# Optimization experiments

Measured on AMD Instinct MI355X. Metric: run time of the kernel, lower is better.

## Reference

```python
import jax, jax.numpy as jnp
import numpy as np

B, N, C = 512, 200, 512
NH, WS = 8, 5  # num_heads, window size (window_size=(5,1), W=1 so w-axis is trivial)
HD = C // NH
SCALE = HD ** -0.5


def setup_inputs() -> dict:
    key = jax.random.key(0)
    k0, k1, k2 = jax.random.split(key, 3)
    std = C ** -0.5
    return {
        "x": jax.random.normal(k0, (B, N, C), dtype=jnp.float32),
        "qkv_w": jax.random.normal(k1, (C, 3 * C), dtype=jnp.float32) * std,
        "qkv_b": jnp.zeros((3 * C,), dtype=jnp.float32),
        "proj_w": jax.random.normal(k2, (C, C), dtype=jnp.float32) * std,
        "proj_b": jnp.zeros((C,), dtype=jnp.float32),
    }


def reference(x, qkv_w, qkv_b, proj_w, proj_b):
    b, n, c = x.shape
    g = n // WS  # number of windows along the 200-token axis (w_group == 1)
    # window partition: since W=1 and window_size[1]=1, partition is a pure reshape
    xw = x.reshape(b * g, WS, c)
    qkv = xw @ qkv_w + qkv_b                      # [b*g, WS, 3C]
    qkv = qkv.reshape(b * g, WS, 3, NH, HD)
    q, k, v = jnp.moveaxis(qkv, 2, 0)             # each [b*g, WS, NH, HD]
    q = jnp.swapaxes(q, 1, 2)                     # [b*g, NH, WS, HD]
    k = jnp.swapaxes(k, 1, 2)
    v = jnp.swapaxes(v, 1, 2)
    attn = jnp.einsum("gnqd,gnkd->gnqk", q, k) * SCALE
    attn = jax.nn.softmax(attn, axis=-1)
    o = jnp.einsum("gnqk,gnkd->gnqd", attn, v)    # [b*g, NH, WS, HD]
    o = jnp.swapaxes(o, 1, 2).reshape(b, n, c)    # window reverse (pure reshape)
    return o @ proj_w + proj_b
```

## Files before the change

kernel.cpp:

```cpp
#include <hip/hip_runtime.h>
#include <stdint.h>


typedef unsigned short u16;
typedef __bf16 bf16_t;
typedef bf16_t bf16x8 __attribute__((ext_vector_type(8)));
typedef float f32x4 __attribute__((ext_vector_type(4)));
typedef u16 u16x8 __attribute__((ext_vector_type(8)));

__device__ __forceinline__ float b2f(u16 u) {
  return __uint_as_float(((uint32_t)u) << 16);
}
__device__ __forceinline__ u16 f2b(float f) {
  uint32_t u = __float_as_uint(f);
  u += 0x7FFFu + ((u >> 16) & 1u);
  return (u16)(u >> 16);
}

#define GLOAD_LDS16(g, l)                                     \
  __builtin_amdgcn_global_load_lds(                           \
      (const __attribute__((address_space(1))) void*)(g),     \
      (__attribute__((address_space(3))) void*)(l), 16, 0, 0)

__global__ void k_sniff_bias(const uint32_t* __restrict__ x,
                             const void* __restrict__ qb,
                             const void* __restrict__ pb,
                             uint32_t* __restrict__ flag,
                             u16* __restrict__ bq, u16* __restrict__ bp) {
  __shared__ uint32_t fsh;
  if (threadIdx.x == 0) {
    int cnt = 0;
    for (int i = 0; i < 256; ++i) {
      uint32_t e = (x[i] >> 23) & 0xFFu;
      if (e >= 64u && e <= 192u) ++cnt;
    }
    uint32_t fl = (cnt >= 128) ? 1u : 0u;
    *flag = fl;
    fsh = fl;
  }
  __syncthreads();
  const bool f = fsh != 0;
  for (int i = threadIdx.x; i < 2048; i += 1024) {
    if (i < 1536)
      bq[i] = f ? f2b(((const float*)qb)[i]) : ((const u16*)qb)[i];
    else {
      int j = i - 1536;
      bp[j] = f ? f2b(((const float*)pb)[j]) : ((const u16*)pb)[j];
    }
  }
}

__global__ void k_prep_w2(const void* __restrict__ qkvw,
                          const void* __restrict__ projw,
                          u16* __restrict__ wq, u16* __restrict__ wp,
                          const uint32_t* __restrict__ flag) {
  __shared__ u16 tile[32][33];
  const bool f = (*flag) != 0;
  int bxi = blockIdx.x;
  const void* in;
  u16* out;
  int Cc;
  if (bxi < 48) {
    in = qkvw; out = wq; Cc = 1536;
  } else {
    bxi -= 48; in = projw; out = wp; Cc = 512;
  }
  const int R = 512;
  const int bx = bxi * 32, by = blockIdx.y * 32;
  const int tx = threadIdx.x, ty = threadIdx.y;
  for (int i = ty; i < 32; i += 8) {
    size_t idx = (size_t)(by + i) * Cc + bx + tx;
    tile[i][tx] = f ? f2b(((const float*)in)[idx]) : ((const u16*)in)[idx];
  }
  __syncthreads();
  for (int i = ty; i < 32; i += 8)
    out[(size_t)(bx + i) * R + by + tx] = tile[tx][i];
}

__global__ void k_conv_x(const float* __restrict__ x, u16* __restrict__ xb,
                         const uint32_t* __restrict__ flag, int n) {
  if ((*flag) == 0) return;
  int i = (blockIdx.x * 256 + threadIdx.x) * 8;
  if (i >= n) return;
  float4 a = *(const float4*)&x[i];
  float4 b = *(const float4*)&x[i + 4];
  u16x8 o;
  o[0] = f2b(a.x); o[1] = f2b(a.y); o[2] = f2b(a.z); o[3] = f2b(a.w);
  o[4] = f2b(b.x); o[5] = f2b(b.y); o[6] = f2b(b.z); o[7] = f2b(b.w);
  *(u16x8*)&xb[i] = o;
}

#define BM 256
#define BN 256

__global__ __launch_bounds__(512, 1) void gemm_bt_bias(
    const u16* __restrict__ A0,
    const u16* __restrict__ A1,
    const u16* __restrict__ Bt, const u16* __restrict__ bias,
    void* __restrict__ Cout, const uint32_t* __restrict__ flag,
    int N, int K, int out_f32_if_flag) {
  __shared__ u16 smem[65536];

  const bool f = (*flag) != 0;
  const u16* A = f ? A1 : A0;

  const int t = threadIdx.x;
  const int wave = t >> 6;
  const int lane = t & 63;
  const int waveM = wave >> 2;
  const int waveN = wave & 3;

  const int nbx = gridDim.x;
  const int nwg = nbx * gridDim.y;
  const int bid = blockIdx.y * nbx + blockIdx.x;
  const int cpx = nwg >> 3;
  const int swz = (bid & 7) * cpx + (bid >> 3);
  const int bm = (swz / nbx) * BM;
  const int bn = (swz % nbx) * BN;

  const int l15 = lane & 15;
  const int rdOff = ((lane >> 5) & 1) * 256 + l15 * 16 + ((lane >> 4) & 1) * 8;
  const int rowS = (lane >> 1) & 15;
  const int colS = ((lane >> 5) & 1) * 16 + (lane & 1) * 8;
  const u16* AgS[4];
  const u16* BgS[4];
#pragma unroll
  for (int q = 0; q < 4; ++q) {
    const int c = wave * 4 + q, g = c >> 1, p = c & 1;
    AgS[q] = &A[(size_t)(bm + g * 16 + rowS) * K + p * 32 + colS];
    BgS[q] = &Bt[(size_t)(bn + g * 16 + rowS) * K + p * 32 + colS];
  }

  f32x4 acc[8][4] = {};
  const int NT = K / 64;

#define STAGE_OP(PTRS, dstU16, kN)                                          \
  {                                                                         \
    _Pragma("unroll") for (int q = 0; q < 4; ++q)                           \
        GLOAD_LDS16(PTRS[q] + (kN), &smem[(dstU16) + (wave * 4 + q) * 512]); \
  }

#define PHASE(MH, NH, STAGECODE, TAILWAIT)                                   \
  {                                                                          \
    bf16x8 af[4][2], bfr[2][2];                                              \
    _Pragma("unroll") for (int ii = 0; ii < 4; ++ii)                         \
        _Pragma("unroll") for (int ks = 0; ks < 2; ++ks)                     \
            af[ii][ks] = *(const bf16x8*)&smem[ab +                          \
                (waveM * 8 + (MH) * 4 + ii) * 1024 + ks * 512 + rdOff];      \
    _Pragma("unroll") for (int jj = 0; jj < 2; ++jj)                         \
        _Pragma("unroll") for (int ks = 0; ks < 2; ++ks)                     \
            bfr[jj][ks] = *(const bf16x8*)&smem[bb +                         \
                (waveN * 4 + (NH) * 2 + jj) * 1024 + ks * 512 + rdOff];      \
    STAGECODE;                                                               \
    asm volatile("" ::: "memory");                                           \
    __builtin_amdgcn_s_barrier();                                            \
    asm volatile("" ::: "memory");                                           \
    __builtin_amdgcn_s_setprio(1);                                           \
    _Pragma("unroll") for (int ii = 0; ii < 4; ++ii)                         \
        _Pragma("unroll") for (int jj = 0; jj < 2; ++jj)                     \
            _Pragma("unroll") for (int ks = 0; ks < 2; ++ks)                 \
                acc[(MH) * 4 + ii][(NH) * 2 + jj] =                          \
                    __builtin_amdgcn_mfma_f32_16x16x32_bf16(                 \
                        af[ii][ks], bfr[jj][ks],                             \
                        acc[(MH) * 4 + ii][(NH) * 2 + jj], 0, 0, 0);         \
    __builtin_amdgcn_s_setprio(0);                                           \
    TAILWAIT;                                                                \
    asm volatile("" ::: "memory");                                           \
    __builtin_amdgcn_s_barrier();                                            \
    asm volatile("" ::: "memory");                                           \
  }

  STAGE_OP(AgS, 0, 0);
  STAGE_OP(BgS, 16384, 0);
  asm volatile("s_waitcnt vmcnt(0)" ::: "memory");
  __builtin_amdgcn_s_barrier();
  asm volatile("" ::: "memory");

  for (int tt = 0; tt < NT; ++tt) {
    const int ab = (tt & 1) * 32768;
    const int bb = ab + 16384;
    const int sab = ((tt + 1) & 1) * 32768;
    const int sbb = sab + 16384;
    const int kN = (tt + 1) * 64;
    const bool st = (tt + 1) < NT;
    PHASE(0, 0, if (st) STAGE_OP(AgS, sab, kN), )
    PHASE(0, 1, if (st) STAGE_OP(BgS, sbb, kN), )
    PHASE(1, 0, , )
    PHASE(1, 1, , asm volatile("s_waitcnt vmcnt(0)" ::: "memory"))
  }
#undef PHASE
#undef STAGE_OP

  __syncthreads();

  float biasf[4];
#pragma unroll
  for (int j = 0; j < 4; ++j)
    biasf[j] = b2f(bias[bn + waveN * 64 + j * 16 + l15]);

  if (out_f32_if_flag && f) {
    float* C = (float*)Cout;
#pragma unroll
    for (int i = 0; i < 8; ++i) {
      const int row0 = waveM * 128 + i * 16 + (lane >> 4) * 4;
#pragma unroll
      for (int j = 0; j < 4; ++j) {
        const int col = waveN * 64 + j * 16 + l15;
#pragma unroll
        for (int r = 0; r < 4; ++r)
          C[(size_t)(bm + row0 + r) * N + bn + col] = acc[i][j][r] + biasf[j];
      }
    }
  } else {
    u16* C = (u16*)Cout;
#pragma unroll
    for (int h = 0; h < 2; ++h) {
      if (waveM == h) {
#pragma unroll
        for (int i = 0; i < 8; ++i) {
          const int row0 = i * 16 + (lane >> 4) * 4;
#pragma unroll
          for (int j = 0; j < 4; ++j) {
            const int col = waveN * 64 + j * 16 + l15;
#pragma unroll
            for (int r = 0; r < 4; ++r)
              smem[(row0 + r) * 256 + col] = f2b(acc[i][j][r] + biasf[j]);
          }
        }
      }
      __syncthreads();
#pragma unroll
      for (int s = 0; s < 8; ++s) {
        const int vi = s * 512 + t;
        const int row = vi >> 5;
        const int col = (vi & 31) * 8;
        u16x8 v = *(const u16x8*)&smem[row * 256 + col];
        *(u16x8*)&C[(size_t)(bm + h * 128 + row) * N + bn + col] = v;
      }
      __syncthreads();
    }
  }
}

__global__ __launch_bounds__(256) void attn_win(const u16* __restrict__ qkv,
                                                u16* __restrict__ o,
                                                int nwin) {
  const int w = blockIdx.x * 4 + (threadIdx.x >> 6);
  if (w >= nwin) return;
  const int lane = threadIdx.x & 63;
  const int h = lane >> 3;
  const int d0 = (lane & 7) * 8;
  const u16* base = qkv + (size_t)w * (5 * 1536) + h * 64 + d0;

  float qf[5][8], kf[5][8], vf[5][8];
#pragma unroll
  for (int i = 0; i < 5; ++i) {
    u16x8 vq = *(const u16x8*)&base[i * 1536];
    u16x8 vk = *(const u16x8*)&base[i * 1536 + 512];
    u16x8 vv = *(const u16x8*)&base[i * 1536 + 1024];
#pragma unroll
    for (int e = 0; e < 8; ++e) {
      qf[i][e] = b2f(vq[e]);
      kf[i][e] = b2f(vk[e]);
      vf[i][e] = b2f(vv[e]);
    }
  }

  float s[5][5];
#pragma unroll
  for (int i = 0; i < 5; ++i)
#pragma unroll
    for (int j = 0; j < 5; ++j) {
      float acc = 0.f;
#pragma unroll
      for (int e = 0; e < 8; ++e) acc += qf[i][e] * kf[j][e];
      s[i][j] = acc;
    }
#pragma unroll
  for (int off = 1; off < 8; off <<= 1) {
#pragma unroll
    for (int i = 0; i < 5; ++i)
#pragma unroll
      for (int j = 0; j < 5; ++j) s[i][j] += __shfl_xor(s[i][j], off, 64);
  }

  const float SCALE = 0.125f;
  u16* ob = o + (size_t)w * (5 * 512) + h * 64 + d0;
#pragma unroll
  for (int i = 0; i < 5; ++i) {
    float m = s[i][0];
#pragma unroll
    for (int j = 1; j < 5; ++j) m = fmaxf(m, s[i][j]);
    float e0[5], l = 0.f;
#pragma unroll
    for (int j = 0; j < 5; ++j) {
      e0[j] = __expf((s[i][j] - m) * SCALE);
      l += e0[j];
    }
    const float rl = 1.f / l;
    u16x8 out;
#pragma unroll
    for (int e = 0; e < 8; ++e) {
      float acc = 0.f;
#pragma unroll
      for (int j = 0; j < 5; ++j) acc += e0[j] * vf[j][e];
      out[e] = f2b(acc * rl);
    }
    *(u16x8*)&ob[i * 512] = out;
  }
}

extern "C" void kernel_launch(void* const* d_in, const int* in_sizes, int n_in,
                              void* d_out, int out_size, void* d_ws,
                              size_t ws_size, hipStream_t stream) {
  const void* x      = d_in[0];
  const void* qkv_w  = d_in[1];
  const void* qkv_b  = d_in[2];
  const void* proj_w = d_in[3];
  const void* proj_b = d_in[4];

  const int M = 102400, K = 512, N1 = 1536, N2 = 512;

  const size_t fixed = 8192 + 1572864 + 524288 + (size_t)M * 512 * 2;
  int CH = 4;
  if (ws_size >= fixed + (size_t)M * 2048 * 2) CH = 1;
  else if (ws_size >= fixed + (size_t)(M / 2) * 2048 * 2) CH = 2;
  const int MC = M / CH;

  char* ws = (char*)d_ws;
  uint32_t* flag = (uint32_t*)ws;
  u16* bq      = (u16*)(ws + 256);
  u16* bp      = (u16*)(ws + 256 + 3072);
  u16* wt_qkv  = (u16*)(ws + 8192);
  u16* wt_proj = (u16*)(ws + 8192 + 1572864);
  u16* attnb   = (u16*)(ws + 8192 + 1572864 + 524288);
  u16* qkvc    = (u16*)((char*)attnb + (size_t)M * 512 * 2);
  u16* xbc     = (u16*)((char*)qkvc + (size_t)MC * 1536 * 2);

  k_sniff_bias<<<1, 1024, 0, stream>>>((const uint32_t*)x, qkv_b, proj_b, flag,
                                       bq, bp);
  k_prep_w2<<<dim3(64, 16), dim3(32, 8), 0, stream>>>(qkv_w, proj_w, wt_qkv,
                                                      wt_proj, flag);
  for (int c = 0; c < CH; ++c) {
    const size_t roff = (size_t)c * MC * 512;
    k_conv_x<<<MC * 512 / 2048, 256, 0, stream>>>((const float*)x + roff, xbc,
                                                  flag, MC * 512);
    gemm_bt_bias<<<dim3(N1 / BN, MC / BM), 512, 0, stream>>>(
        (const u16*)x + roff, xbc, wt_qkv, bq, qkvc, flag, N1, K, 0);
    attn_win<<<(MC / 5) / 4, 256, 0, stream>>>(qkvc, (u16*)attnb + roff,
                                               MC / 5);
  }
  gemm_bt_bias<<<dim3(N2 / BN, M / BM), 512, 0, stream>>>(
      attnb, attnb, wt_proj, bp, d_out, flag, N2, K, 1);
}
```

Measured before the change: 768.7 us.

## Replace four-phase barrier schedule with single-barrier loop and fragment reuse

Drops the four PHASE blocks, each with two barriers and an s_setprio bump, that interleaved global-to-LDS staging with MFMA groups. Each k-tile now issues both A and B prefetches up front, loads A/B fragments in a snake order so they are reused across quadrants, and uses a single __syncthreads per tile. This cuts barrier count and redundant LDS reads of fragments. In exchange, the compiler handles waitcnt placement and loses explicit wave priority control, so load/compute overlap may get worse.

```diff
diff --git a/kernel.cpp b/kernel.cpp
--- a/kernel.cpp
+++ b/kernel.cpp
@@ -140,58 +140,79 @@
         GLOAD_LDS16(PTRS[q] + (kN), &smem[(dstU16) + (wave * 4 + q) * 512]); \
   }
 
-#define PHASE(MH, NH, STAGECODE, TAILWAIT)                                   \
-  {                                                                          \
-    bf16x8 af[4][2], bfr[2][2];                                              \
-    _Pragma("unroll") for (int ii = 0; ii < 4; ++ii)                         \
-        _Pragma("unroll") for (int ks = 0; ks < 2; ++ks)                     \
-            af[ii][ks] = *(const bf16x8*)&smem[ab +                          \
-                (waveM * 8 + (MH) * 4 + ii) * 1024 + ks * 512 + rdOff];      \
-    _Pragma("unroll") for (int jj = 0; jj < 2; ++jj)                         \
-        _Pragma("unroll") for (int ks = 0; ks < 2; ++ks)                     \
-            bfr[jj][ks] = *(const bf16x8*)&smem[bb +                         \
-                (waveN * 4 + (NH) * 2 + jj) * 1024 + ks * 512 + rdOff];      \
-    STAGECODE;                                                               \
-    asm volatile("" ::: "memory");                                           \
-    __builtin_amdgcn_s_barrier();                                            \
-    asm volatile("" ::: "memory");                                           \
-    __builtin_amdgcn_s_setprio(1);                                           \
-    _Pragma("unroll") for (int ii = 0; ii < 4; ++ii)                         \
-        _Pragma("unroll") for (int jj = 0; jj < 2; ++jj)                     \
-            _Pragma("unroll") for (int ks = 0; ks < 2; ++ks)                 \
-                acc[(MH) * 4 + ii][(NH) * 2 + jj] =                          \
-                    __builtin_amdgcn_mfma_f32_16x16x32_bf16(                 \
-                        af[ii][ks], bfr[jj][ks],                             \
-                        acc[(MH) * 4 + ii][(NH) * 2 + jj], 0, 0, 0);         \
-    __builtin_amdgcn_s_setprio(0);                                           \
-    TAILWAIT;                                                                \
-    asm volatile("" ::: "memory");                                           \
-    __builtin_amdgcn_s_barrier();                                            \
-    asm volatile("" ::: "memory");                                           \
-  }
-
   STAGE_OP(AgS, 0, 0);
   STAGE_OP(BgS, 16384, 0);
-  asm volatile("s_waitcnt vmcnt(0)" ::: "memory");
-  __builtin_amdgcn_s_barrier();
-  asm volatile("" ::: "memory");
+  __syncthreads();
 
   for (int tt = 0; tt < NT; ++tt) {
     const int ab = (tt & 1) * 32768;
     const int bb = ab + 16384;
-    const int sab = ((tt + 1) & 1) * 32768;
-    const int sbb = sab + 16384;
-    const int kN = (tt + 1) * 64;
-    const bool st = (tt + 1) < NT;
-    PHASE(0, 0, if (st) STAGE_OP(AgS, sab, kN), )
-    PHASE(0, 1, if (st) STAGE_OP(BgS, sbb, kN), )
-    PHASE(1, 0, , )
-    PHASE(1, 1, , asm volatile("s_waitcnt vmcnt(0)" ::: "memory"))
-  }
-#undef PHASE
+    if (tt + 1 < NT) {
+      const int sab = ((tt + 1) & 1) * 32768;
+      const int kN = (tt + 1) * 64;
+      STAGE_OP(AgS, sab, kN);
+      STAGE_OP(BgS, sab + 16384, kN);
+    }
+    bf16x8 a0[4][2], a1[4][2], b0[2][2], b1[2][2];
+#pragma unroll
+    for (int ii = 0; ii < 4; ++ii)
+#pragma unroll
+      for (int ks = 0; ks < 2; ++ks)
+        a0[ii][ks] = *(const bf16x8*)&smem[ab + (waveM * 8 + ii) * 1024 +
+                                           ks * 512 + rdOff];
+#pragma unroll
+    for (int jj = 0; jj < 2; ++jj)
+#pragma unroll
+      for (int ks = 0; ks < 2; ++ks)
+        b0[jj][ks] = *(const bf16x8*)&smem[bb + (waveN * 4 + jj) * 1024 +
+                                           ks * 512 + rdOff];
+#pragma unroll
+    for (int ii = 0; ii < 4; ++ii)
+#pragma unroll
+      for (int jj = 0; jj < 2; ++jj)
+#pragma unroll
+        for (int ks = 0; ks < 2; ++ks)
+          acc[ii][jj] = __builtin_amdgcn_mfma_f32_16x16x32_bf16(
+              a0[ii][ks], b0[jj][ks], acc[ii][jj], 0, 0, 0);
+#pragma unroll
+    for (int jj = 0; jj < 2; ++jj)
+#pragma unroll
+      for (int ks = 0; ks < 2; ++ks)
+        b1[jj][ks] = *(const bf16x8*)&smem[bb + (waveN * 4 + 2 + jj) * 1024 +
+                                           ks * 512 + rdOff];
+#pragma unroll
+    for (int ii = 0; ii < 4; ++ii)
+#pragma unroll
+      for (int jj = 0; jj < 2; ++jj)
+#pragma unroll
+        for (int ks = 0; ks < 2; ++ks)
+          acc[ii][2 + jj] = __builtin_amdgcn_mfma_f32_16x16x32_bf16(
+              a0[ii][ks], b1[jj][ks], acc[ii][2 + jj], 0, 0, 0);
+#pragma unroll
+    for (int ii = 0; ii < 4; ++ii)
+#pragma unroll
+      for (int ks = 0; ks < 2; ++ks)
+        a1[ii][ks] = *(const bf16x8*)&smem[ab + (waveM * 8 + 4 + ii) * 1024 +
+                                           ks * 512 + rdOff];
+#pragma unroll
+    for (int ii = 0; ii < 4; ++ii)
+#pragma unroll
+      for (int jj = 0; jj < 2; ++jj)
+#pragma unroll
+        for (int ks = 0; ks < 2; ++ks)
+          acc[4 + ii][2 + jj] = __builtin_amdgcn_mfma_f32_16x16x32_bf16(
+              a1[ii][ks], b1[jj][ks], acc[4 + ii][2 + jj], 0, 0, 0);
+#pragma unroll
+    for (int ii = 0; ii < 4; ++ii)
+#pragma unroll
+      for (int jj = 0; jj < 2; ++jj)
+#pragma unroll
+        for (int ks = 0; ks < 2; ++ks)
+          acc[4 + ii][jj] = __builtin_amdgcn_mfma_f32_16x16x32_bf16(
+              a1[ii][ks], b0[jj][ks], acc[4 + ii][jj], 0, 0, 0);
+    __syncthreads();
+  }
 #undef STAGE_OP
-
-  __syncthreads();
 
   float biasf[4];
 #pragma unroll
```

After: 772.2 us. No clear change (+0.5%).
